# Kernel tuning notes

Measured on AMD Instinct MI355X. Metric: run time of the kernel, lower is better.

## Reference

```python
import jax, jax.numpy as jnp
import numpy as np

D_MODEL = 256
N_HEADS = 8
HEAD_DIM = D_MODEL // N_HEADS  # 32
N_LEVELS = 4
N_POINTS = 4
LEVEL_SHAPES = [(100, 100), (50, 50), (25, 25), (13, 13)]
LEVEL_STARTS = [0] + list(np.cumsum([h * w for h, w in LEVEL_SHAPES]))[:-1]
LEN_IN = int(sum(h * w for h, w in LEVEL_SHAPES))  # 13294
BATCH = 2
LEN_Q = LEN_IN  # encoder self-attention


def _offset_bias():
    # faithful to MSDeformAttn._reset_parameters for sampling_offsets bias
    thetas = np.arange(N_HEADS, dtype=np.float32) * (2.0 * np.pi / N_HEADS)
    grid = np.stack([np.cos(thetas), np.sin(thetas)], -1)
    grid = grid / np.abs(grid).max(-1, keepdims=True)
    grid = np.tile(grid.reshape(N_HEADS, 1, 1, 2), (1, N_LEVELS, N_POINTS, 1))
    for i in range(N_POINTS):
        grid[:, :, i, :] *= i + 1
    return jnp.asarray(grid.reshape(-1), dtype=jnp.float32)


def setup_inputs() -> dict:
    key = jax.random.key(0)
    ks = jax.random.split(key, 10)
    s = 1.0 / np.sqrt(D_MODEL)
    inp = {
        "query": jax.random.normal(ks[0], (BATCH, LEN_Q, D_MODEL), jnp.float32),
        "reference_points": jax.random.uniform(ks[1], (BATCH, LEN_Q, N_LEVELS, 2), jnp.float32),
        "input_flatten": jax.random.normal(ks[2], (BATCH, LEN_IN, D_MODEL), jnp.float32),
        "input_spatial_shapes": jnp.asarray(LEVEL_SHAPES, dtype=jnp.int32),
        "W_value": jax.random.normal(ks[3], (D_MODEL, D_MODEL), jnp.float32) * s,
        "b_value": jnp.zeros((D_MODEL,), jnp.float32),
        "W_off": jax.random.normal(ks[4], (D_MODEL, N_HEADS * N_LEVELS * N_POINTS * 2), jnp.float32) * 0.01,
        "b_off": _offset_bias(),
        "W_attn": jax.random.normal(ks[5], (D_MODEL, N_HEADS * N_LEVELS * N_POINTS), jnp.float32) * 0.01,
        "b_attn": jnp.zeros((N_HEADS * N_LEVELS * N_POINTS,), jnp.float32),
        "W_out": jax.random.normal(ks[6], (D_MODEL, D_MODEL), jnp.float32) * s,
        "b_out": jnp.zeros((D_MODEL,), jnp.float32),
    }
    return inp


def _corner(v_t, ix, iy, h, w):
    # v_t: (n, M, h*w, D); ix/iy: (n, M, LqP) int32. Zero padding outside.
    valid = (ix >= 0) & (ix < w) & (iy >= 0) & (iy < h)
    idx = jnp.clip(iy, 0, h - 1) * w + jnp.clip(ix, 0, w - 1)
    g = jnp.take_along_axis(v_t, idx[..., None], axis=2)  # (n, M, LqP, D)
    return g * valid[..., None].astype(v_t.dtype)


def _ms_deform_attn(query, reference_points, input_flatten,
                    W_value, b_value, W_off, b_off, W_attn, b_attn, W_out, b_out):
    n, lq, _ = query.shape
    value = (input_flatten @ W_value + b_value).reshape(n, LEN_IN, N_HEADS, HEAD_DIM)
    offs = (query @ W_off + b_off).reshape(n, lq, N_HEADS, N_LEVELS, N_POINTS, 2)
    aw = jax.nn.softmax(
        (query @ W_attn + b_attn).reshape(n, lq, N_HEADS, N_LEVELS * N_POINTS), axis=-1
    ).reshape(n, lq, N_HEADS, N_LEVELS, N_POINTS)
    # offset_normalizer = (w, h) per level
    norm = jnp.asarray([[w, h] for h, w in LEVEL_SHAPES], dtype=query.dtype)
    loc = reference_points[:, :, None, :, None, :] + offs / norm[None, None, None, :, None, :]

    acc = jnp.zeros((n, N_HEADS, lq, HEAD_DIM), dtype=value.dtype)
    for l, (h, w) in enumerate(LEVEL_SHAPES):
        s0 = LEVEL_STARTS[l]
        v_t = jnp.transpose(value[:, s0:s0 + h * w], (0, 2, 1, 3))  # (n, M, hw, D)
        ll = loc[:, :, :, l]  # (n, lq, M, P, 2) in [0,1]
        # grid_sample bilinear, align_corners=False: pixel = coord*size - 0.5
        x = ll[..., 0] * w - 0.5
        y = ll[..., 1] * h - 0.5
        x0 = jnp.floor(x); y0 = jnp.floor(y)
        tx = x - x0; ty = y - y0
        ix0 = x0.astype(jnp.int32); iy0 = y0.astype(jnp.int32)
        flat = lambda a: jnp.transpose(a, (0, 2, 1, 3)).reshape(n, N_HEADS, lq * N_POINTS)
        ix0f, iy0f = flat(ix0), flat(iy0)
        txf = flat(tx)[..., None]; tyf = flat(ty)[..., None]
        g00 = _corner(v_t, ix0f, iy0f, h, w)
        g01 = _corner(v_t, ix0f + 1, iy0f, h, w)
        g10 = _corner(v_t, ix0f, iy0f + 1, h, w)
        g11 = _corner(v_t, ix0f + 1, iy0f + 1, h, w)
        samp = (g00 * (1 - txf) * (1 - tyf) + g01 * txf * (1 - tyf)
                + g10 * (1 - txf) * tyf + g11 * txf * tyf)
        samp = samp.reshape(n, N_HEADS, lq, N_POINTS, HEAD_DIM)
        wl = jnp.transpose(aw[:, :, :, l], (0, 2, 1, 3))[..., None]  # (n, M, lq, P, 1)
        acc = acc + (samp * wl).sum(axis=3)

    out = jnp.transpose(acc, (0, 2, 1, 3)).reshape(n, lq, D_MODEL)
    return out @ W_out + b_out


def reference(query, reference_points, input_flatten, input_spatial_shapes,
              W_value, b_value, W_off, b_off, W_attn, b_attn, W_out, b_out):
    # input_spatial_shapes carried for signature fidelity; level geometry is static.
    return _ms_deform_attn(query, reference_points, input_flatten,
                           W_value, b_value, W_off, b_off, W_attn, b_attn, W_out, b_out)
```

## Files before the change

kernel.cpp:

```cpp
#include <hip/hip_runtime.h>

#define NH 8
#define HD 32
#define NL 4
#define NP 4
#define DM 256
#define LEN_IN_C 13294
#define LQ_C 13294
#define B_C 2
#define M_TOTAL (B_C * LQ_C)
#define MT_TILES 1662
#define GQ 32
#define QBLKS 831
#define LROWB 1040

typedef __attribute__((ext_vector_type(8))) short short8;
typedef __attribute__((ext_vector_type(4))) float floatx4;

__device__ __forceinline__ unsigned short f2bf(float x) {
    union { float f; unsigned int u; } a; a.f = x;
    unsigned int r = (a.u + 0x7FFFu + ((a.u >> 16) & 1u)) >> 16;
    return (unsigned short)r;
}
__device__ __forceinline__ unsigned short f2h(float x) {
    unsigned int r;
    asm("v_cvt_f16_f32 %0, %1" : "=v"(r) : "v"(x));
    return (unsigned short)r;
}
__device__ __forceinline__ unsigned int cvtpk_bf16(float lo, float hi) {
    unsigned int r;
    asm("v_cvt_pk_bf16_f32 %0, %1, %2" : "=v"(r) : "v"(lo), "v"(hi));
    return r;
}

#define FMAMIX_LO(acc, v, w) \
    asm("v_fma_mix_f32 %0, %1, %2, %0 op_sel_hi:[1,0,0]" : "+v"(acc) : "v"(v), "v"(w))
#define FMAMIX_HI(acc, v, w) \
    asm("v_fma_mix_f32 %0, %1, %2, %0 op_sel:[1,0,0] op_sel_hi:[1,0,0]" : "+v"(acc) : "v"(v), "v"(w))

__device__ __forceinline__ void dma16(const float* g, float* l) {
    __builtin_amdgcn_global_load_lds(
        (const __attribute__((address_space(1))) unsigned int*)(g),
        (__attribute__((address_space(3))) unsigned int*)(l), 16, 0, 0);
}

__device__ __forceinline__ void conv_b_body(const float* __restrict__ W,
                                            unsigned short* __restrict__ Bsw,
                                            int Nsrc, int NTsrc, int NTtotal, int ntOff,
                                            int vblk) {
    const int u = vblk * 256 + threadIdx.x;
    const int lane = u & 63;
    const int unit = u >> 6;
    const int ntl = unit % NTsrc;
    const int kc = unit / NTsrc;
    const int n = ntl * 16 + (lane & 15);
    const int k0 = kc * 32 + (lane >> 4) * 8;
    short8 v;
#pragma unroll
    for (int j = 0; j < 8; ++j)
        v[j] = (short)f2bf(W[(size_t)(k0 + j) * Nsrc + n]);
    ((short8*)Bsw)[(size_t)(kc * NTtotal + ntOff + ntl) * 64 + lane] = v;
}

__global__ __launch_bounds__(256) void conv_weights_kernel(const float* __restrict__ Wv,
                                                           const float* __restrict__ Woff,
                                                           const float* __restrict__ Wattn,
                                                           const float* __restrict__ Wout,
                                                           unsigned short* __restrict__ BswV,
                                                           unsigned short* __restrict__ BswH,
                                                           unsigned short* __restrict__ BswO,
                                                           unsigned short* __restrict__ value,
                                                           unsigned short* __restrict__ AccSw) {
    const int blk = blockIdx.x;
    if (blk < 32)        conv_b_body(Wv,    BswV,  256, 16, 16, 0,  blk);
    else if (blk < 80) {
        const int u = (blk - 32) * 256 + threadIdx.x;
        const int lane = u & 63;
        const int unit = u >> 6;
        const int h = unit / 24;
        const int rem = unit % 24;
        const int kc = rem / 3;
        const int ntl = rem % 3;
        const int colq = lane & 15;
        const int k0 = kc * 32 + (lane >> 4) * 8;
        const float* W = (ntl < 2) ? Woff : Wattn;
        const int Nsrc = (ntl < 2) ? 256 : 128;
        const int n = (ntl < 2) ? (h * 32 + ntl * 16 + colq) : (h * 16 + colq);
        short8 v;
#pragma unroll
        for (int j = 0; j < 8; ++j)
            v[j] = (short)f2bf(W[(size_t)(k0 + j) * Nsrc + n]);
        ((short8*)BswH)[(size_t)unit * 64 + lane] = v;
    }
    else if (blk < 112)  conv_b_body(Wout, BswO, 256, 16, 16, 0, blk - 80);
    else if (blk < 113) {
        const int t = threadIdx.x;
        if (t < 32) {
            value[-32 + t] = 0;
            value[(size_t)M_TOTAL * 256 + t] = 0;
        }
    } else {
        const int idx = threadIdx.x;
        if (idx < 128) {
            const int kc = idx >> 4;
            const int sub = idx & 15;
            const int lane = (12 + (sub & 3)) + 16 * (sub >> 2);
            const size_t unit = (size_t)(1661 * 8 + kc) * 64 + lane;
            short8 z = (short8){0, 0, 0, 0, 0, 0, 0, 0};
            ((short8*)AccSw)[unit] = z;
        }
    }
}

__global__ __launch_bounds__(256) void front_gemm_kernel(const float* __restrict__ inflat,
                                                         const unsigned short* __restrict__ BswV,
                                                         const float* __restrict__ bv,
                                                         unsigned short* __restrict__ value, int M) {
    __shared__ float sA[16 * LROWB / 4];
    const int tid = threadIdx.x;
    const int lane = tid & 63;
    const int wave = tid >> 6;
    const int trow = blockIdx.x * 16;

#pragma unroll
    for (int i = 0; i < 4; ++i) {
        const int lrow = i * 4 + wave;
        const int srow = min(trow + lrow, M - 1);
        dma16(inflat + (size_t)srow * 256 + lane * 4,
              (float*)((char*)sA + lrow * LROWB));
    }
    __syncthreads();

    const int m = lane & 15;
    const int q = lane >> 4;
    const short8* Bu = (const short8*)BswV;

    floatx4 acc[4];
#pragma unroll
    for (int t = 0; t < 4; ++t) acc[t] = (floatx4){0.f, 0.f, 0.f, 0.f};

#pragma unroll 2
    for (int kc = 0; kc < 8; ++kc) {
        const char* fb = (const char*)sA + m * LROWB + kc * 128 + q * 32;
        const float4 f0 = *(const float4*)fb;
        const float4 f1 = *(const float4*)(fb + 16);
        union { uint4 u; short8 s; } c;
        c.u.x = cvtpk_bf16(f0.x, f0.y); c.u.y = cvtpk_bf16(f0.z, f0.w);
        c.u.z = cvtpk_bf16(f1.x, f1.y); c.u.w = cvtpk_bf16(f1.z, f1.w);
        const short8 a = c.s;
#pragma unroll
        for (int t = 0; t < 4; ++t) {
            const short8 b = Bu[(size_t)(kc * 16 + wave * 4 + t) * 64 + lane];
            acc[t] = __builtin_amdgcn_mfma_f32_16x16x32_bf16(a, b, acc[t], 0, 0, 0);
        }
    }

    const int colq = lane & 15;
    const int rowq = (lane >> 4) * 4;
#pragma unroll
    for (int t = 0; t < 4; ++t) {
        const int col = (wave * 4 + t) * 16 + colq;
        const float bc = bv[col];
#pragma unroll
        for (int reg = 0; reg < 4; ++reg) {
            const int row = trow + rowq + reg;
            if (row < M) {
                const float v = acc[t][reg] + bc;
                const int bb = row >= LEN_IN_C;
                const int pos = row - (bb ? LEN_IN_C : 0);
                const int hh = col >> 5;
                const int dd = col & 31;
                value[((size_t)((bb << 3) + hh) * LEN_IN_C + pos) * 32 + dd] = f2h(v);
            }
        }
    }
}

__global__ __launch_bounds__(256) void back_gemm_kernel(const unsigned short* __restrict__ Asw,
                                                        const unsigned short* __restrict__ Bsw,
                                                        const float* __restrict__ bias,
                                                        float* __restrict__ Cout, int M) {
    const int tid = threadIdx.x;
    const int lane = tid & 63;
    const int wave = tid >> 6;
    const int x = blockIdx.x;
    const int rt = x >> 1;
    const int half = x & 1;
    const int nt0 = half * 8 + wave * 2;

    const short8* Au = (const short8*)Asw;
    const short8* Bu = (const short8*)Bsw;

    floatx4 acc[2];
    acc[0] = (floatx4){0.f, 0.f, 0.f, 0.f};
    acc[1] = acc[0];

#pragma unroll 2
    for (int kc = 0; kc < 8; ++kc) {
        const short8 a = Au[(size_t)(rt * 8 + kc) * 64 + lane];
#pragma unroll
        for (int t = 0; t < 2; ++t) {
            const short8 b = Bu[(size_t)(kc * 16 + nt0 + t) * 64 + lane];
            acc[t] = __builtin_amdgcn_mfma_f32_16x16x32_bf16(a, b, acc[t], 0, 0, 0);
        }
    }

    const int colq = lane & 15;
    const int rowq = (lane >> 4) * 4;
#pragma unroll
    for (int t = 0; t < 2; ++t) {
        const int col = (nt0 + t) * 16 + colq;
        const float bc = bias[col];
#pragma unroll
        for (int reg = 0; reg < 4; ++reg) {
            const int row = rt * 16 + rowq + reg;
            if (row < M)
                Cout[(size_t)row * 256 + col] = acc[t][reg] + bc;
        }
    }
}

__global__ __launch_bounds__(256, 4) void msda_fused_kernel(const float* __restrict__ refp,
                                                            const float* __restrict__ query,
                                                            const unsigned short* __restrict__ value,
                                                            const unsigned short* __restrict__ BswH,
                                                            const float* __restrict__ boff,
                                                            const float* __restrict__ battn,
                                                            unsigned short* __restrict__ AccSw) {
    constexpr int lvl_hw[4] = {100, 50, 25, 13};
    constexpr int lvl_s[4] = {0, 10000, 12500, 13125};

    const int wg = blockIdx.x;
    const int h = wg & 7;
    const int q0 = (wg >> 3) * GQ;
    const int tid = threadIdx.x;
    const int lane = tid & 63;
    const int wave = tid >> 6;

    __shared__ float s_ref[GQ * 8];
    __shared__ float s_fused[GQ][50];
    __shared__ __attribute__((aligned(16))) char s_mix[17408];
    uint4* s_pdb = (uint4*)s_mix;

    s_ref[tid] = refp[min(q0 * 8 + tid, M_TOTAL * 8 - 1)];

#pragma unroll
    for (int i = 0; i < 8; ++i) {
        const int li = i * 1024 + tid * 4;
        const int lrow = li >> 8;
        const int lcol = li & 255;
        const int srow = min(q0 + lrow, M_TOTAL - 1);
        const float4 f = *(const float4*)(query + (size_t)srow * 256 + lcol);
        uint2 pk;
        pk.x = cvtpk_bf16(f.x, f.y);
        pk.y = cvtpk_bf16(f.z, f.w);
        *(uint2*)(s_mix + ((li * 2) ^ ((lrow & 7) << 4))) = pk;
    }
    __syncthreads();

    {
        const int m = lane & 15;
        const int q = lane >> 4;
        const int swz = (m & 7) << 4;
        const short8* Bu = (const short8*)BswH;
        const int colq = lane & 15;
        const int rowq = (lane >> 4) * 4;
#pragma unroll
        for (int pass = 0; pass < 2; ++pass) {
            const int i = wave + pass * 4;
            if (i < 6) {
                const int r = i & 1;
                const int ct = i >> 1;
                floatx4 acc = (floatx4){0.f, 0.f, 0.f, 0.f};
#pragma unroll
                for (int kc = 0; kc < 8; ++kc) {
                    const short8 a = *(const short8*)(s_mix +
                        (((m + r * 16) * 512 + kc * 64 + q * 16) ^ swz));
                    const short8 b = Bu[(size_t)(h * 24 + kc * 3 + ct) * 64 + lane];
                    acc = __builtin_amdgcn_mfma_f32_16x16x32_bf16(a, b, acc, 0, 0, 0);
                }
                const float bc = (ct < 2) ? boff[h * 32 + ct * 16 + colq]
                                          : battn[h * 16 + colq];
#pragma unroll
                for (int reg = 0; reg < 4; ++reg)
                    s_fused[r * 16 + rowq + reg][ct * 16 + colq] = acc[reg] + bc;
            }
        }
    }
    __syncthreads();

#pragma unroll
    for (int jj = 0; jj < 2; ++jj) {
        const int job = jj * 256 + tid;
        const int qq = job >> 4;
        const int t16 = job & 15;
        const int l = t16 >> 2;
        const int bq = min(q0 + qq, M_TOTAL - 1);
        const int b = (bq >= LQ_C) ? 1 : 0;

        const float logit = s_fused[qq][32 + t16];
        float m = logit;
#pragma unroll
        for (int mask = 1; mask < 16; mask <<= 1) m = fmaxf(m, __shfl_xor(m, mask));
        const float e = __expf(logit - m);
        float s = e;
#pragma unroll
        for (int mask = 1; mask < 16; mask <<= 1) s += __shfl_xor(s, mask);
        const float aw = e / s;

        const int whl = lvl_hw[l];
        const float fwh = (float)whl;
        const float ox = s_fused[qq][t16 * 2];
        const float oy = s_fused[qq][t16 * 2 + 1];
        const float x = s_ref[qq * 8 + l * 2] * fwh + ox - 0.5f;
        const float y = s_ref[qq * 8 + l * 2 + 1] * fwh + oy - 0.5f;
        const float x0f = floorf(x), y0f = floorf(y);
        const float tx = x - x0f, ty = y - y0f;
        const int ix0 = (int)x0f, iy0 = (int)y0f;

        const bool xv0 = (unsigned)ix0 < (unsigned)whl;
        const bool xv1 = (unsigned)(ix0 + 1) < (unsigned)whl;
        const bool yv0 = (unsigned)iy0 < (unsigned)whl;
        const bool yv1 = (unsigned)(iy0 + 1) < (unsigned)whl;

        const int cxp = min(max(ix0, -1), whl - 1);
        const int cy0 = min(max(iy0, 0), whl - 1);
        const int cy1 = min(max(iy0 + 1, 0), whl - 1);

        const int posb = (b * 8 + h) * LEN_IN_C + lvl_s[l];
        const int offT = (posb + cy0 * whl + cxp) * 64;
        const int offB = (posb + cy1 * whl + cxp) * 64;
        const float w00 = (xv0 && yv0) ? aw * (1.f - tx) * (1.f - ty) : 0.f;
        const float w01 = (xv1 && yv0) ? aw * tx * (1.f - ty) : 0.f;
        const float w10 = (xv0 && yv1) ? aw * (1.f - tx) * ty : 0.f;
        const float w11 = (xv1 && yv1) ? aw * tx * ty : 0.f;
        const int slot = qq * 17 + t16;
        uint4 d0, d1;
        d0.x = (unsigned)offT; d0.y = (unsigned)offB;
        d0.z = __float_as_uint(w00); d0.w = __float_as_uint(w10);
        d1.x = (unsigned)offT; d1.y = (unsigned)offB;
        d1.z = __float_as_uint(w01); d1.w = __float_as_uint(w11);
        s_pdb[slot] = d0;
        s_pdb[GQ * 17 + slot] = d1;
    }
    __syncthreads();

    const int qq = tid >> 3;
    const int l8 = tid & 7;
    const char* vbp = (const char*)value + l8 * 16;
    const int side = (l8 >> 2) & 1;
    const uint4* pd = s_pdb + side * (GQ * 17) + qq * 17;

    float a0 = 0.f, a1 = 0.f, a2 = 0.f, a3 = 0.f;
    float a4 = 0.f, a5 = 0.f, a6 = 0.f, a7 = 0.f;
#pragma unroll 2
    for (int pt = 0; pt < 16; ++pt) {
        const uint4 d = pd[pt];
        const float wt = __uint_as_float(d.z);
        const float wb = __uint_as_float(d.w);
        const uint4 vt = *(const uint4*)(vbp + (int)d.x);
        const uint4 vb = *(const uint4*)(vbp + (int)d.y);
        FMAMIX_LO(a0, vt.x, wt); FMAMIX_HI(a1, vt.x, wt);
        FMAMIX_LO(a2, vt.y, wt); FMAMIX_HI(a3, vt.y, wt);
        FMAMIX_LO(a4, vt.z, wt); FMAMIX_HI(a5, vt.z, wt);
        FMAMIX_LO(a6, vt.w, wt); FMAMIX_HI(a7, vt.w, wt);
        FMAMIX_LO(a0, vb.x, wb); FMAMIX_HI(a1, vb.x, wb);
        FMAMIX_LO(a2, vb.y, wb); FMAMIX_HI(a3, vb.y, wb);
        FMAMIX_LO(a4, vb.z, wb); FMAMIX_HI(a5, vb.z, wb);
        FMAMIX_LO(a6, vb.w, wb); FMAMIX_HI(a7, vb.w, wb);
    }

    a0 += __shfl_xor(a0, 4); a1 += __shfl_xor(a1, 4);
    a2 += __shfl_xor(a2, 4); a3 += __shfl_xor(a3, 4);
    a4 += __shfl_xor(a4, 4); a5 += __shfl_xor(a5, 4);
    a6 += __shfl_xor(a6, 4); a7 += __shfl_xor(a7, 4);

    const int bq = q0 + qq;
    if (side == 0 && bq < M_TOTAL) {
        const int rt = bq >> 4, mm = bq & 15;
        const int unit = (rt * 8 + h) * 64 + ((l8 & 3) * 16 + mm);
        uint4 o;
        o.x = cvtpk_bf16(a0, a1);
        o.y = cvtpk_bf16(a2, a3);
        o.z = cvtpk_bf16(a4, a5);
        o.w = cvtpk_bf16(a6, a7);
        *(uint4*)(AccSw + (size_t)unit * 8) = o;
    }
}

extern "C" void kernel_launch(void* const* d_in, const int* in_sizes, int n_in,
                              void* d_out, int out_size, void* d_ws, size_t ws_size,
                              hipStream_t stream) {
    const float* query  = (const float*)d_in[0];
    const float* refp   = (const float*)d_in[1];
    const float* inflat = (const float*)d_in[2];
    const float* Wv    = (const float*)d_in[4];
    const float* bv    = (const float*)d_in[5];
    const float* Woff  = (const float*)d_in[6];
    const float* boff  = (const float*)d_in[7];
    const float* Wattn = (const float*)d_in[8];
    const float* battn = (const float*)d_in[9];
    const float* Wout  = (const float*)d_in[10];
    const float* bout  = (const float*)d_in[11];
    float* out = (float*)d_out;

    char* p = (char*)d_ws;
    unsigned short* AccSw = (unsigned short*)p;
    p += (size_t)MT_TILES * 8 * 64 * 8 * sizeof(unsigned short);
    unsigned short* BswV = (unsigned short*)p;   p += (size_t)8 * 16 * 64 * 8 * 2;
    unsigned short* BswH = (unsigned short*)p;   p += (size_t)192 * 64 * 8 * 2;
    unsigned short* BswO = (unsigned short*)p;   p += (size_t)8 * 16 * 64 * 8 * 2;
    unsigned short* value = (unsigned short*)p + 32;
    p += ((size_t)M_TOTAL * 256 + 64) * sizeof(unsigned short);

    const int M = M_TOTAL;

    conv_weights_kernel<<<114, 256, 0, stream>>>(Wv, Woff, Wattn, Wout,
                                                 BswV, BswH, BswO, value, AccSw);
    front_gemm_kernel<<<MT_TILES, 256, 0, stream>>>(inflat, BswV, bv, value, M);
    msda_fused_kernel<<<QBLKS * 8, 256, 0, stream>>>(refp, query, value, BswH,
                                                     boff, battn, AccSw);
    back_gemm_kernel<<<MT_TILES * 2, 256, 0, stream>>>(AccSw, BswO, bout, out, M);
}
```

Baseline: 193.8 us.

## Precompute swizzled bf16 query once and raise fused kernel occupancy

Adds a kernel that converts the fp32 query into a bf16 MFMA fragment layout in workspace once. The fused deformable-attention kernel then loads A fragments directly from global memory instead of having every head's workgroup reload and convert the query tile into LDS. This removes the 8x redundant query conversion and a block-wide barrier, and the launch bound is raised to allow more resident workgroups. The cost is an extra kernel launch plus an extra workspace write and read of the converted query.

New measurement: 200.1 us. +3.2%, slower.

```diff
diff --git a/kernel.cpp b/kernel.cpp
--- a/kernel.cpp
+++ b/kernel.cpp
@@ -42,6 +42,29 @@
     __builtin_amdgcn_global_load_lds(
         (const __attribute__((address_space(1))) unsigned int*)(g),
         (__attribute__((address_space(3))) unsigned int*)(l), 16, 0, 0);
+}
+
+__global__ __launch_bounds__(256) void conv_a_kernel(const float* __restrict__ A,
+                                                     unsigned short* __restrict__ Asw,
+                                                     int M) {
+    const int u = blockIdx.x * 256 + threadIdx.x;
+    const int lane = u & 63;
+    const int kc = (u >> 6) & 7;
+    const int rt = u >> 9;
+    const int row = rt * 16 + (lane & 15);
+    const int col0 = kc * 32 + (lane >> 4) * 8;
+    short8 v;
+    if (row < M) {
+        const float4 f0 = *(const float4*)(A + (size_t)row * 256 + col0);
+        const float4 f1 = *(const float4*)(A + (size_t)row * 256 + col0 + 4);
+        union { uint4 u4; short8 s; } c;
+        c.u4.x = cvtpk_bf16(f0.x, f0.y); c.u4.y = cvtpk_bf16(f0.z, f0.w);
+        c.u4.z = cvtpk_bf16(f1.x, f1.y); c.u4.w = cvtpk_bf16(f1.z, f1.w);
+        v = c.s;
+    } else {
+        v = (short8){0, 0, 0, 0, 0, 0, 0, 0};
+    }
+    ((short8*)Asw)[u] = v;
 }
 
 __device__ __forceinline__ void conv_b_body(const float* __restrict__ W,
@@ -220,8 +243,8 @@
     }
 }
 
-__global__ __launch_bounds__(256, 4) void msda_fused_kernel(const float* __restrict__ refp,
-                                                            const float* __restrict__ query,
+__global__ __launch_bounds__(256, 6) void msda_fused_kernel(const float* __restrict__ refp,
+                                                            const unsigned short* __restrict__ AswQ,
                                                             const unsigned short* __restrict__ value,
                                                             const unsigned short* __restrict__ BswH,
                                                             const float* __restrict__ boff,
@@ -233,35 +256,19 @@
     const int wg = blockIdx.x;
     const int h = wg & 7;
     const int q0 = (wg >> 3) * GQ;
+    const int rt0 = (wg >> 3) * 2;
     const int tid = threadIdx.x;
     const int lane = tid & 63;
     const int wave = tid >> 6;
 
     __shared__ float s_ref[GQ * 8];
     __shared__ float s_fused[GQ][50];
-    __shared__ __attribute__((aligned(16))) char s_mix[17408];
-    uint4* s_pdb = (uint4*)s_mix;
+    __shared__ uint4 s_pdb[2 * GQ * 17];
 
     s_ref[tid] = refp[min(q0 * 8 + tid, M_TOTAL * 8 - 1)];
 
-#pragma unroll
-    for (int i = 0; i < 8; ++i) {
-        const int li = i * 1024 + tid * 4;
-        const int lrow = li >> 8;
-        const int lcol = li & 255;
-        const int srow = min(q0 + lrow, M_TOTAL - 1);
-        const float4 f = *(const float4*)(query + (size_t)srow * 256 + lcol);
-        uint2 pk;
-        pk.x = cvtpk_bf16(f.x, f.y);
-        pk.y = cvtpk_bf16(f.z, f.w);
-        *(uint2*)(s_mix + ((li * 2) ^ ((lrow & 7) << 4))) = pk;
-    }
-    __syncthreads();
-
     {
-        const int m = lane & 15;
-        const int q = lane >> 4;
-        const int swz = (m & 7) << 4;
+        const short8* AuQ = (const short8*)AswQ;
         const short8* Bu = (const short8*)BswH;
         const int colq = lane & 15;
         const int rowq = (lane >> 4) * 4;
@@ -274,8 +281,7 @@
                 floatx4 acc = (floatx4){0.f, 0.f, 0.f, 0.f};
 #pragma unroll
                 for (int kc = 0; kc < 8; ++kc) {
-                    const short8 a = *(const short8*)(s_mix +
-                        (((m + r * 16) * 512 + kc * 64 + q * 16) ^ swz));
+                    const short8 a = AuQ[(size_t)((rt0 + r) * 8 + kc) * 64 + lane];
                     const short8 b = Bu[(size_t)(h * 24 + kc * 3 + ct) * 64 + lane];
                     acc = __builtin_amdgcn_mfma_f32_16x16x32_bf16(a, b, acc, 0, 0, 0);
                 }
@@ -407,6 +413,8 @@
     char* p = (char*)d_ws;
     unsigned short* AccSw = (unsigned short*)p;
     p += (size_t)MT_TILES * 8 * 64 * 8 * sizeof(unsigned short);
+    unsigned short* AswQ = (unsigned short*)p;
+    p += (size_t)MT_TILES * 8 * 64 * 8 * sizeof(unsigned short);
     unsigned short* BswV = (unsigned short*)p;   p += (size_t)8 * 16 * 64 * 8 * 2;
     unsigned short* BswH = (unsigned short*)p;   p += (size_t)192 * 64 * 8 * 2;
     unsigned short* BswO = (unsigned short*)p;   p += (size_t)8 * 16 * 64 * 8 * 2;
@@ -417,8 +425,9 @@
 
     conv_weights_kernel<<<114, 256, 0, stream>>>(Wv, Woff, Wattn, Wout,
                                                  BswV, BswH, BswO, value, AccSw);
+    conv_a_kernel<<<MT_TILES * 2, 256, 0, stream>>>(query, AswQ, M);
     front_gemm_kernel<<<MT_TILES, 256, 0, stream>>>(inflat, BswV, bv, value, M);
-    msda_fused_kernel<<<QBLKS * 8, 256, 0, stream>>>(refp, query, value, BswH,
+    msda_fused_kernel<<<QBLKS * 8, 256, 0, stream>>>(refp, AswQ, value, BswH,
                                                      boff, battn, AccSw);
     back_gemm_kernel<<<MT_TILES * 2, 256, 0, stream>>>(AccSw, BswO, bout, out, M);
 }
```
